# Kernel optimization log

Hardware: AMD Instinct MI355X
Metric: run time of the kernel (lower is better)

The kernel has to match this reference:

```python
import jax, jax.numpy as jnp
import numpy as np

B, S, D, H = 2, 2048, 1024, 16
DK = D // H

def setup_inputs() -> dict:
    key = jax.random.key(0)
    ks = jax.random.split(key, 12)
    s = 1.0 / np.sqrt(D)
    return {
        "q": jax.random.normal(ks[0], (B, S, D), jnp.float32),
        "k": jax.random.normal(ks[1], (B, S, D), jnp.float32),
        "v": jax.random.normal(ks[2], (B, S, D), jnp.float32),
        "mask": jnp.ones((1, 1, S, S), jnp.int32),
        "Wq": jax.random.normal(ks[3], (D, D), jnp.float32) * s,
        "bq": jnp.zeros((D,), jnp.float32),
        "Wk": jax.random.normal(ks[4], (D, D), jnp.float32) * s,
        "bk": jnp.zeros((D,), jnp.float32),
        "Wv": jax.random.normal(ks[5], (D, D), jnp.float32) * s,
        "bv": jnp.zeros((D,), jnp.float32),
        "Wo": jax.random.normal(ks[6], (D, D), jnp.float32) * s,
        "bo": jnp.zeros((D,), jnp.float32),
    }

def reference(q, k, v, mask, Wq, bq, Wk, bk, Wv, bv, Wo, bo):
    # projections (torch Linear: x @ W^T + b)
    Q = q @ Wq.T + bq
    K = k @ Wk.T + bk
    V = v @ Wv.T + bv
    # split heads: [B,S,D] -> [B,H,S,DK]
    def split(x):
        return x.reshape(B, S, H, DK).transpose(0, 2, 1, 3)
    Qh, Kh, Vh = split(Q), split(K), split(V)
    scores = jnp.einsum('bhqd,bhkd->bhqk', Qh, Kh) / jnp.sqrt(jnp.float32(DK))
    scores = jnp.where(mask == 0, jnp.float32(-1e9), scores)
    attn = jax.nn.softmax(scores, axis=-1)  # dropout p=0.0 -> identity
    x = jnp.einsum('bhqk,bhkd->bhqd', attn, Vh)
    x = x.transpose(0, 2, 1, 3).reshape(B, S, D)
    return x @ Wo.T + bo
```

## Files before the change

kernel.cpp:

```cpp
#include <hip/hip_runtime.h>
#include <hip/hip_bf16.h>
#include <stdint.h>

#define B_    2
#define S_    2048
#define D_    1024
#define H_    16
#define NTOK  (B_ * S_)

typedef __attribute__((ext_vector_type(8))) short bf16x8;
typedef __attribute__((ext_vector_type(4))) float f32x4;
typedef __attribute__((ext_vector_type(2))) float float2v;
typedef __attribute__((ext_vector_type(2))) __bf16 bfv2;

static __device__ __forceinline__ unsigned int pkbf(float a, float b) {
    float2v fv = {a, b};
    bfv2 r = __builtin_convertvector(fv, bfv2);
    unsigned int u;
    __builtin_memcpy(&u, &r, 4);
    return u;
}

using g_cu32 = __attribute__((address_space(1))) const unsigned int;
using l_u32  = __attribute__((address_space(3))) unsigned int;
static __device__ __forceinline__ void gld16(const void* g, void* l) {
    __builtin_amdgcn_global_load_lds((g_cu32*)g, (l_u32*)l, 16, 0, 0);
}

#define QN ((size_t)NTOK * D_)
#define WN ((size_t)D_ * D_)

struct SwapT { static constexpr bool value = true; };
struct NoSwapT { static constexpr bool value = false; };

__global__ __launch_bounds__(256) void prep_kernel(
    const float* __restrict__ q, const float* __restrict__ k, const float* __restrict__ v,
    const float* __restrict__ Wq, const float* __restrict__ Wk,
    const float* __restrict__ Wv, const float* __restrict__ Wo,
    const int* __restrict__ mask,
    unsigned short* __restrict__ qb, unsigned short* __restrict__ kb,
    unsigned short* __restrict__ vb, unsigned short* __restrict__ wqb,
    unsigned short* __restrict__ wkb, unsigned short* __restrict__ wvb,
    unsigned short* __restrict__ wob, int* __restrict__ flags) {
    __shared__ int anyz;
    if (blockIdx.x < 8192) {
        size_t i = ((size_t)blockIdx.x * 256 + threadIdx.x) * 8;
        const float* s; unsigned short* d; size_t off;
        if (i < QN)          { s = q; d = qb; off = i; }
        else if (i < 2 * QN) { s = k; d = kb; off = i - QN; }
        else if (i < 3 * QN) { s = v; d = vb; off = i - 2 * QN; }
        else {
            size_t j = i - 3 * QN;
            int wi = (int)(j >> 20);
            s = (wi == 0) ? Wq : (wi == 1) ? Wk : (wi == 2) ? Wv : Wo;
            d = (wi == 0) ? wqb : (wi == 1) ? wkb : (wi == 2) ? wvb : wob;
            off = j & (WN - 1);
        }
        float4 a = *(const float4*)(s + off);
        float4 b = *(const float4*)(s + off + 4);
        uint4 pk;
        pk.x = pkbf(a.x, a.y); pk.y = pkbf(a.z, a.w);
        pk.z = pkbf(b.x, b.y); pk.w = pkbf(b.z, b.w);
        *(uint4*)(d + off) = pk;
    } else {
        if (threadIdx.x == 0) anyz = 0;
        __syncthreads();
        int bid2 = blockIdx.x - 8192;
        const int qt = bid2 >> 5, kt = bid2 & 31;
        int az = 0;
        for (int i = threadIdx.x; i < 64 * 64; i += 256) {
            int r = i >> 6, c = i & 63;
            az |= (mask[(size_t)(qt * 64 + r) * S_ + kt * 64 + c] == 0) ? 1 : 0;
        }
        if (az) atomicOr(&anyz, 1);
        __syncthreads();
        if (threadIdx.x == 0) flags[qt * 32 + kt] = anyz;
    }
}

struct GemmArgs {
    const unsigned short* A[3];
    const unsigned short* W[3];
    const float* bias[3];
    void* C[3];
    int mode[3];
    float scale[3];
};

template<int BMT>
__global__ __launch_bounds__(256, 3) void gemm_async(GemmArgs ga) {
    constexpr int AG = BMT / 16;
    constexpr int MI = BMT / 32;
    const int z = blockIdx.z;
    const unsigned short* __restrict__ A = ga.A[z];
    const unsigned short* __restrict__ W = ga.W[z];
    const float* __restrict__ bias = ga.bias[z];
    void* C = ga.C[z];
    const int mode = ga.mode[z];
    const float scl = ga.scale[z];

    __shared__ unsigned short As[AG * 512];
    __shared__ unsigned short Bs[8 * 512];

    const int t    = threadIdx.x;
    const int lane = t & 63;
    const int w    = t >> 6;
    const int fr   = lane & 15;
    const int kq   = lane >> 4;
    const int wrow = w >> 1, wcol = w & 1;
    const int m0 = blockIdx.x * BMT, n0 = blockIdx.y * 128;

    const int sc = lane >> 4;
    const int sr = lane & 15;

    const unsigned short* ga0;
    const unsigned short* ga1 = nullptr;
    unsigned short* la0;
    unsigned short* la1 = nullptr;
    if constexpr (BMT == 128) {
        ga0 = A + (size_t)(m0 + (2 * w) * 16 + sr) * D_ + sc * 8;
        ga1 = ga0 + 16 * D_;
        la0 = &As[(2 * w) * 512];
        la1 = &As[(2 * w + 1) * 512];
    } else {
        ga0 = A + (size_t)(m0 + w * 16 + sr) * D_ + sc * 8;
        la0 = &As[w * 512];
    }
    const unsigned short* gw0 = W + (size_t)(n0 + (2 * w) * 16 + sr) * D_ + sc * 8;
    const unsigned short* gw1 = gw0 + 16 * D_;
    unsigned short* lw0 = &Bs[(2 * w) * 512];
    unsigned short* lw1 = &Bs[(2 * w + 1) * 512];

    int aOff[MI], bOff[4];
#pragma unroll
    for (int mi = 0; mi < MI; ++mi) aOff[mi] = (wrow * MI + mi) * 512 + (kq * 16 + fr) * 8;
#pragma unroll
    for (int ni = 0; ni < 4; ++ni) bOff[ni] = (wcol * 4 + ni) * 512 + (kq * 16 + fr) * 8;

    f32x4 acc[MI][4];
#pragma unroll
    for (int i = 0; i < MI; ++i)
#pragma unroll
        for (int j = 0; j < 4; ++j) acc[i][j] = (f32x4)0.0f;

    auto kloop = [&](auto swc) {
        constexpr bool SW = decltype(swc)::value;
        for (int k0 = 0; k0 < D_ / 32; ++k0) {
            gld16(ga0, la0);
            if constexpr (BMT == 128) gld16(ga1, la1);
            gld16(gw0, lw0);
            gld16(gw1, lw1);
            ga0 += 32; gw0 += 32; gw1 += 32;
            if constexpr (BMT == 128) ga1 += 32;
            __syncthreads();

            bf16x8 af[MI], bfr[4];
#pragma unroll
            for (int mi = 0; mi < MI; ++mi) af[mi] = *(const bf16x8*)&As[aOff[mi]];
#pragma unroll
            for (int ni = 0; ni < 4; ++ni) bfr[ni] = *(const bf16x8*)&Bs[bOff[ni]];
#pragma unroll
            for (int mi = 0; mi < MI; ++mi)
#pragma unroll
                for (int ni = 0; ni < 4; ++ni) {
                    if constexpr (SW)
                        acc[mi][ni] = __builtin_amdgcn_mfma_f32_16x16x32_bf16(
                            bfr[ni], af[mi], acc[mi][ni], 0, 0, 0);
                    else
                        acc[mi][ni] = __builtin_amdgcn_mfma_f32_16x16x32_bf16(
                            af[mi], bfr[ni], acc[mi][ni], 0, 0, 0);
                }
            __syncthreads();
        }
    };
    if (mode == 2) kloop(NoSwapT{}); else kloop(SwapT{});

    if (mode == 2) {
        unsigned short* Co = (unsigned short*)C;
#pragma unroll
        for (int ni = 0; ni < 4; ++ni) {
            int col = n0 + wcol * 64 + ni * 16 + fr;
            float bv = bias[col];
            int hh = col >> 6, d = col & 63;
#pragma unroll
            for (int mi = 0; mi < MI; ++mi) {
                int tok = m0 + wrow * (BMT / 2) + mi * 16 + kq * 4;
                int bb = tok >> 11, sbase = tok & (S_ - 1);
                uint2 pk;
                pk.x = pkbf((acc[mi][ni][0] + bv) * scl, (acc[mi][ni][1] + bv) * scl);
                pk.y = pkbf((acc[mi][ni][2] + bv) * scl, (acc[mi][ni][3] + bv) * scl);
                *(uint2*)(Co + ((size_t)((bb * H_ + hh) * 64 + d)) * S_ + sbase) = pk;
            }
        }
    } else if (mode == 0) {
        float* Co = (float*)C;
#pragma unroll
        for (int ni = 0; ni < 4; ++ni) {
            int nb = n0 + wcol * 64 + ni * 16 + kq * 4;
            float4 b4 = *(const float4*)&bias[nb];
#pragma unroll
            for (int mi = 0; mi < MI; ++mi) {
                int m = m0 + wrow * (BMT / 2) + mi * 16 + fr;
                float4 o4;
                o4.x = (acc[mi][ni][0] + b4.x) * scl;
                o4.y = (acc[mi][ni][1] + b4.y) * scl;
                o4.z = (acc[mi][ni][2] + b4.z) * scl;
                o4.w = (acc[mi][ni][3] + b4.w) * scl;
                *(float4*)(Co + (size_t)m * D_ + nb) = o4;
            }
        }
    } else {
        unsigned short* Co = (unsigned short*)C;
#pragma unroll
        for (int ni = 0; ni < 4; ++ni) {
            int nb = n0 + wcol * 64 + ni * 16 + kq * 4;
            float4 b4 = *(const float4*)&bias[nb];
#pragma unroll
            for (int mi = 0; mi < MI; ++mi) {
                int m = m0 + wrow * (BMT / 2) + mi * 16 + fr;
                uint2 pk;
                pk.x = pkbf((acc[mi][ni][0] + b4.x) * scl, (acc[mi][ni][1] + b4.y) * scl);
                pk.y = pkbf((acc[mi][ni][2] + b4.z) * scl, (acc[mi][ni][3] + b4.w) * scl);
                *(uint2*)(Co + (size_t)m * D_ + nb) = pk;
            }
        }
    }
}

__global__ __launch_bounds__(512, 4) void flash4(
    const unsigned short* __restrict__ Qb, const unsigned short* __restrict__ Kb,
    const unsigned short* __restrict__ Vtg, const int* __restrict__ mask,
    const int* __restrict__ flags, unsigned short* __restrict__ Xb) {
    __shared__ unsigned short Ks[2][4096];
    __shared__ unsigned short Vs[2][4096];
    __shared__ unsigned short Ps[8192];

    const int t    = threadIdx.x;
    const int lane = t & 63;
    const int w    = t >> 6;
    const int fr   = lane & 15;
    const int kq   = lane >> 4;
    const int bid = blockIdx.x;
    const int swb = ((bid & 7) << 6) | (bid >> 3);
    const int qt = swb & 15, hd = (swb >> 4) & 15, b = swb >> 8;
    const int q0 = qt * 128;
    const int swz = fr & 7;

    const unsigned short* qrow_p = Qb + (size_t)(b * S_ + q0 + w * 16 + fr) * D_ + hd * 64;
    bf16x8 qf[2];
    qf[0] = *(const bf16x8*)(qrow_p + kq * 8);
    qf[1] = *(const bf16x8*)(qrow_p + 32 + kq * 8);

    int fl = (lane < 32) ? flags[(qt * 2 + (w >> 2)) * 32 + lane] : 0;
    unsigned int fmask = (unsigned int)__ballot(fl != 0);

    const unsigned short* kptr =
        Kb + (size_t)(b * S_ + (w >> 1) * 16 + fr) * D_ + hd * 64 + (w & 1) * 32 + kq * 8;
    const unsigned short* vptr =
        Vtg + ((size_t)((b * H_ + hd) * 64 + (w >> 1) * 16 + fr)) * S_ + (w & 1) * 32 + kq * 8;

    gld16(kptr, (char*)&Ks[0][0] + w * 1024);
    gld16(vptr, (char*)&Vs[0][0] + w * 1024);
    const unsigned short* kpf = kptr + (size_t)64 * D_;
    const unsigned short* vpf = vptr + 64;

    unsigned short* pswr[4];
#pragma unroll
    for (int mi = 0; mi < 4; ++mi) {
        int chunk = mi * 2 + (kq >> 1);
        pswr[mi] = &Ps[(w * 16 + fr) * 64 + ((chunk ^ swz) << 3) + ((kq & 1) << 2)];
    }
    const unsigned short* psrd[2];
#pragma unroll
    for (int kk = 0; kk < 2; ++kk) {
        int c = kk * 4 + kq;
        psrd[kk] = &Ps[(w * 16 + fr) * 64 + ((c ^ swz) << 3)];
    }

    const f32x4 zf = (f32x4)0.0f;
    f32x4 o[4];
#pragma unroll
    for (int i = 0; i < 4; ++i) o[i] = zf;
    float2v l2 = {0.0f, 0.0f};

    for (int kt = 0; kt < 32; ++kt) {
        const int cur = kt & 1;
        __syncthreads();
        if (kt < 31) {
            gld16(kpf, (char*)&Ks[cur ^ 1][0] + w * 1024);
            gld16(vpf, (char*)&Vs[cur ^ 1][0] + w * 1024);
            kpf += (size_t)64 * D_;
            vpf += 64;
        }

        f32x4 st[4];
#pragma unroll
        for (int mi = 0; mi < 4; ++mi) {
            bf16x8 a = *(const bf16x8*)&Ks[cur][mi * 1024 + (kq * 16 + fr) * 8];
            st[mi] = __builtin_amdgcn_mfma_f32_16x16x32_bf16(a, qf[0], zf, 0, 0, 0);
        }
#pragma unroll
        for (int mi = 0; mi < 4; ++mi) {
            bf16x8 a = *(const bf16x8*)&Ks[cur][mi * 1024 + ((4 + kq) * 16 + fr) * 8];
            st[mi] = __builtin_amdgcn_mfma_f32_16x16x32_bf16(a, qf[1], st[mi], 0, 0, 0);
        }

        if ((fmask >> kt) & 1u) {
#pragma unroll
            for (int mi = 0; mi < 4; ++mi) {
                int4 mv = *(const int4*)&mask[(size_t)(q0 + w * 16 + fr) * S_ + kt * 64 + mi * 16 + kq * 4];
                if (mv.x == 0) st[mi][0] = -3e8f;
                if (mv.y == 0) st[mi][1] = -3e8f;
                if (mv.z == 0) st[mi][2] = -3e8f;
                if (mv.w == 0) st[mi][3] = -3e8f;
            }
        }

#pragma unroll
        for (int mi = 0; mi < 4; ++mi) {
            float e0 = __builtin_amdgcn_exp2f(st[mi][0]);
            float e1 = __builtin_amdgcn_exp2f(st[mi][1]);
            float e2 = __builtin_amdgcn_exp2f(st[mi][2]);
            float e3 = __builtin_amdgcn_exp2f(st[mi][3]);
            l2 += (float2v){e0, e1} + (float2v){e2, e3};
            uint2 pk;
            pk.x = pkbf(e0, e1);
            pk.y = pkbf(e2, e3);
            *(uint2*)pswr[mi] = pk;
        }

#pragma unroll
        for (int kk = 0; kk < 2; ++kk) {
            bf16x8 pb = *(const bf16x8*)psrd[kk];
#pragma unroll
            for (int mi = 0; mi < 4; ++mi) {
                bf16x8 a = *(const bf16x8*)&Vs[cur][mi * 1024 + ((kk * 4 + kq) * 16 + fr) * 8];
                o[mi] = __builtin_amdgcn_mfma_f32_16x16x32_bf16(a, pb, o[mi], 0, 0, 0);
            }
        }
    }

    float l_i = l2.x + l2.y;
    l_i += __shfl_xor(l_i, 16, 64);
    l_i += __shfl_xor(l_i, 32, 64);
    float rl = 1.0f / l_i;

#pragma unroll
    for (int mi = 0; mi < 4; ++mi) {
        uint2 pk;
        pk.x = pkbf(o[mi][0] * rl, o[mi][1] * rl);
        pk.y = pkbf(o[mi][2] * rl, o[mi][3] * rl);
        *(uint2*)(Xb + (size_t)(b * S_ + q0 + w * 16 + fr) * D_ + hd * 64 + mi * 16 + kq * 4) = pk;
    }
}

extern "C" void kernel_launch(void* const* d_in, const int* in_sizes, int n_in,
                              void* d_out, int out_size, void* d_ws, size_t ws_size,
                              hipStream_t stream) {
    const float* q    = (const float*)d_in[0];
    const float* k    = (const float*)d_in[1];
    const float* v    = (const float*)d_in[2];
    const int*   mask = (const int*)d_in[3];
    const float* Wq   = (const float*)d_in[4];
    const float* bq   = (const float*)d_in[5];
    const float* Wk   = (const float*)d_in[6];
    const float* bk   = (const float*)d_in[7];
    const float* Wv   = (const float*)d_in[8];
    const float* bv   = (const float*)d_in[9];
    const float* Wo   = (const float*)d_in[10];
    const float* bo   = (const float*)d_in[11];
    float* out = (float*)d_out;

    unsigned short* qb  = (unsigned short*)d_ws;
    unsigned short* kb  = qb + QN;
    unsigned short* vb  = kb + QN;
    unsigned short* Qf  = vb + QN;
    unsigned short* Kf  = Qf + QN;
    unsigned short* Vt  = Kf + QN;
    unsigned short* wqb = Vt + QN;
    unsigned short* wkb = wqb + WN;
    unsigned short* wvb = wkb + WN;
    unsigned short* wob = wvb + WN;
    int* flags = (int*)(wob + WN);

    const float SC = 0.18033688011112042f;

    prep_kernel<<<9216, 256, 0, stream>>>(q, k, v, Wq, Wk, Wv, Wo, mask,
                                          qb, kb, vb, wqb, wkb, wvb, wob, flags);

    GemmArgs g1;
    g1.A[0] = qb;  g1.W[0] = wqb; g1.bias[0] = bq; g1.C[0] = Qf; g1.mode[0] = 1; g1.scale[0] = SC;
    g1.A[1] = kb;  g1.W[1] = wkb; g1.bias[1] = bk; g1.C[1] = Kf; g1.mode[1] = 1; g1.scale[1] = 1.0f;
    g1.A[2] = vb;  g1.W[2] = wvb; g1.bias[2] = bv; g1.C[2] = Vt; g1.mode[2] = 2; g1.scale[2] = 1.0f;
    gemm_async<128><<<dim3(NTOK / 128, D_ / 128, 3), 256, 0, stream>>>(g1);

    flash4<<<dim3((S_ / 128) * H_ * B_, 1, 1), 512, 0, stream>>>(Qf, Kf, Vt, mask, flags, Qf);

    GemmArgs g2;
    g2.A[0] = Qf; g2.W[0] = wob; g2.bias[0] = bo; g2.C[0] = out; g2.mode[0] = 0; g2.scale[0] = 1.0f;
    g2.A[1] = g2.A[2] = nullptr; g2.W[1] = g2.W[2] = nullptr;
    g2.bias[1] = g2.bias[2] = nullptr; g2.C[1] = g2.C[2] = nullptr;
    g2.mode[1] = g2.mode[2] = 0; g2.scale[1] = g2.scale[2] = 1.0f;
    gemm_async<64><<<dim3(NTOK / 64, D_ / 128, 1), 256, 0, stream>>>(g2);
}
```

Before: 261.2 us.

## Double-buffer LDS tiles in projection GEMM to overlap loads with MFMA

```diff
diff --git a/kernel.cpp b/kernel.cpp
--- a/kernel.cpp
+++ b/kernel.cpp
@@ -91,6 +91,7 @@
 __global__ __launch_bounds__(256, 3) void gemm_async(GemmArgs ga) {
     constexpr int AG = BMT / 16;
     constexpr int MI = BMT / 32;
+    constexpr int NK = D_ / 32;
     const int z = blockIdx.z;
     const unsigned short* __restrict__ A = ga.A[z];
     const unsigned short* __restrict__ W = ga.W[z];
@@ -99,8 +100,8 @@
     const int mode = ga.mode[z];
     const float scl = ga.scale[z];
 
-    __shared__ unsigned short As[AG * 512];
-    __shared__ unsigned short Bs[8 * 512];
+    __shared__ unsigned short As[2][AG * 512];
+    __shared__ unsigned short Bs[2][8 * 512];
 
     const int t    = threadIdx.x;
     const int lane = t & 63;
@@ -115,21 +116,20 @@
 
     const unsigned short* ga0;
     const unsigned short* ga1 = nullptr;
-    unsigned short* la0;
-    unsigned short* la1 = nullptr;
+    int la0Off, la1Off = 0;
     if constexpr (BMT == 128) {
         ga0 = A + (size_t)(m0 + (2 * w) * 16 + sr) * D_ + sc * 8;
         ga1 = ga0 + 16 * D_;
-        la0 = &As[(2 * w) * 512];
-        la1 = &As[(2 * w + 1) * 512];
+        la0Off = (2 * w) * 512;
+        la1Off = (2 * w + 1) * 512;
     } else {
         ga0 = A + (size_t)(m0 + w * 16 + sr) * D_ + sc * 8;
-        la0 = &As[w * 512];
+        la0Off = w * 512;
     }
     const unsigned short* gw0 = W + (size_t)(n0 + (2 * w) * 16 + sr) * D_ + sc * 8;
     const unsigned short* gw1 = gw0 + 16 * D_;
-    unsigned short* lw0 = &Bs[(2 * w) * 512];
-    unsigned short* lw1 = &Bs[(2 * w + 1) * 512];
+    const int lw0Off = (2 * w) * 512;
+    const int lw1Off = (2 * w + 1) * 512;
 
     int aOff[MI], bOff[4];
 #pragma unroll
@@ -142,23 +142,29 @@
     for (int i = 0; i < MI; ++i)
 #pragma unroll
         for (int j = 0; j < 4; ++j) acc[i][j] = (f32x4)0.0f;
+
+    auto stage = [&](int buf) {
+        gld16(ga0, &As[buf][la0Off]);
+        if constexpr (BMT == 128) gld16(ga1, &As[buf][la1Off]);
+        gld16(gw0, &Bs[buf][lw0Off]);
+        gld16(gw1, &Bs[buf][lw1Off]);
+        ga0 += 32; gw0 += 32; gw1 += 32;
+        if constexpr (BMT == 128) ga1 += 32;
+    };
 
     auto kloop = [&](auto swc) {
         constexpr bool SW = decltype(swc)::value;
-        for (int k0 = 0; k0 < D_ / 32; ++k0) {
-            gld16(ga0, la0);
-            if constexpr (BMT == 128) gld16(ga1, la1);
-            gld16(gw0, lw0);
-            gld16(gw1, lw1);
-            ga0 += 32; gw0 += 32; gw1 += 32;
-            if constexpr (BMT == 128) ga1 += 32;
+        stage(0);
+        for (int k0 = 0; k0 < NK; ++k0) {
+            const int cur = k0 & 1;
             __syncthreads();
+            if (k0 < NK - 1) stage(cur ^ 1);
 
             bf16x8 af[MI], bfr[4];
 #pragma unroll
-            for (int mi = 0; mi < MI; ++mi) af[mi] = *(const bf16x8*)&As[aOff[mi]];
-#pragma unroll
-            for (int ni = 0; ni < 4; ++ni) bfr[ni] = *(const bf16x8*)&Bs[bOff[ni]];
+            for (int mi = 0; mi < MI; ++mi) af[mi] = *(const bf16x8*)&As[cur][aOff[mi]];
+#pragma unroll
+            for (int ni = 0; ni < 4; ++ni) bfr[ni] = *(const bf16x8*)&Bs[cur][bOff[ni]];
 #pragma unroll
             for (int mi = 0; mi < MI; ++mi)
 #pragma unroll
@@ -170,7 +176,6 @@
                         acc[mi][ni] = __builtin_amdgcn_mfma_f32_16x16x32_bf16(
                             af[mi], bfr[ni], acc[mi][ni], 0, 0, 0);
                 }
-            __syncthreads();
         }
     };
     if (mode == 2) kloop(NoSwapT{}); else kloop(SwapT{});
```

New measurement: 263.2 us. No clear change (+0.7%).
